# Optimization experiments

Hardware: AMD Instinct MI355X
Metric: run time of the kernel (lower is better)

Reference implementation:

```python
import jax, jax.numpy as jnp
import numpy as np

N, E, B, D, DEPTH = 20000, 160000, 16, 128, 5
L = 4 * DEPTH  # 20 EGNN layer calls: (ground, ground_to_sub, sub, sub_to_ground) x depth


def _ln(x, g, b):
    mu = jnp.mean(x, -1, keepdims=True)
    var = jnp.mean((x - mu) ** 2, -1, keepdims=True)
    return (x - mu) * jax.lax.rsqrt(var + 1e-5) * g + b


def setup_inputs() -> dict:
    key = jax.random.key(0)
    ks = jax.random.split(key, 24)

    def w(k, shape, fan_in):
        return jax.random.normal(k, shape, jnp.float32) / np.float32(np.sqrt(fan_in))

    return {
        "x": jax.random.normal(ks[0], (N, 1), jnp.float32),
        "pos": jax.random.normal(ks[1], (N, 3), jnp.float32),
        "edge_index": jax.random.randint(ks[2], (2, E), 0, N),
        "node_subnode_index": jax.random.randint(ks[3], (2, E), 0, N),
        "subgraph_edge_index": jax.random.randint(ks[4], (2, E), 0, N),
        "subnode_node_index": jax.random.randint(ks[5], (2, E), 0, N),
        "batch_ids": jnp.sort(jax.random.randint(ks[6], (N,), 0, B)),
        "emb_W": w(ks[7], (1, D), 1), "emb_b": jnp.zeros((D,), jnp.float32),
        # message MLP: Linear(2D+1,D) -> LN -> SiLU -> Linear(D,D) -> LN -> SiLU, stacked over L layers
        "Wm1": w(ks[8], (L, 2 * D + 1, D), 2 * D + 1), "bm1": jnp.zeros((L, D), jnp.float32),
        "gm1": jnp.ones((L, D), jnp.float32), "sm1": jnp.zeros((L, D), jnp.float32),
        "Wm2": w(ks[9], (L, D, D), D), "bm2": jnp.zeros((L, D), jnp.float32),
        "gm2": jnp.ones((L, D), jnp.float32), "sm2": jnp.zeros((L, D), jnp.float32),
        # update MLP: Linear(2D,D) -> LN -> SiLU -> Linear(D,D) -> LN -> SiLU
        "Wu1": w(ks[10], (L, 2 * D, D), 2 * D), "bu1": jnp.zeros((L, D), jnp.float32),
        "gu1": jnp.ones((L, D), jnp.float32), "su1": jnp.zeros((L, D), jnp.float32),
        "Wu2": w(ks[11], (L, D, D), D), "bu2": jnp.zeros((L, D), jnp.float32),
        "gu2": jnp.ones((L, D), jnp.float32), "su2": jnp.zeros((L, D), jnp.float32),
        # prediction head: Linear(D,D) -> ReLU -> Linear(D,1)
        "pred_W1": w(ks[12], (D, D), D), "pred_b1": jnp.zeros((D,), jnp.float32),
        "pred_W2": w(ks[13], (D, 1), D), "pred_b2": jnp.zeros((1,), jnp.float32),
    }


def _egnn(h, pos, ei, i, Wm1, bm1, gm1, sm1, Wm2, bm2, gm2, sm2,
          Wu1, bu1, gu1, su1, Wu2, bu2, gu2, su2):
    src, dst = ei[0], ei[1]          # PyG: messages flow source -> target
    rel = pos[dst] - pos[src]
    dist = jnp.sqrt(jnp.sum(rel * rel, -1, keepdims=True))  # [E,1]
    m = jnp.concatenate([h[dst], h[src], dist], -1)          # [E, 2D+1] = [h_i, h_j, d]
    m = jax.nn.silu(_ln(m @ Wm1[i] + bm1[i], gm1[i], sm1[i]))
    m = jax.nn.silu(_ln(m @ Wm2[i] + bm2[i], gm2[i], sm2[i]))
    agg = jax.ops.segment_sum(m, dst, num_segments=h.shape[0])
    u = jnp.concatenate([h, agg], -1)                        # [N, 2D]
    u = jax.nn.silu(_ln(u @ Wu1[i] + bu1[i], gu1[i], su1[i]))
    u = jax.nn.silu(_ln(u @ Wu2[i] + bu2[i], gu2[i], su2[i]))
    return u


def reference(x, pos, edge_index, node_subnode_index, subgraph_edge_index,
              subnode_node_index, batch_ids, emb_W, emb_b,
              Wm1, bm1, gm1, sm1, Wm2, bm2, gm2, sm2,
              Wu1, bu1, gu1, su1, Wu2, bu2, gu2, su2,
              pred_W1, pred_b1, pred_W2, pred_b2):
    p = (Wm1, bm1, gm1, sm1, Wm2, bm2, gm2, sm2,
         Wu1, bu1, gu1, su1, Wu2, bu2, gu2, su2)
    h = x @ emb_W + emb_b
    edge_sets = (edge_index, node_subnode_index, subgraph_edge_index, subnode_node_index)
    for layer_idx in range(DEPTH):
        h0 = h
        for r, ei in enumerate(edge_sets):
            h = _egnn(h, pos, ei, layer_idx * 4 + r, *p)
        h = h + h0  # residual across the 4 message-passing steps
    out = jax.ops.segment_sum(h, batch_ids, num_segments=B)  # global_add_pool
    return jax.nn.relu(out @ pred_W1 + pred_b1) @ pred_W2 + pred_b2
```

## Files before the change

### kernel.cpp

```cpp
#include <hip/hip_runtime.h>

#define NN 20000
#define NE 160000
#define NL 20

typedef float f32x4 __attribute__((ext_vector_type(4)));
typedef float f32x2 __attribute__((ext_vector_type(2)));
typedef __bf16 bf16x8 __attribute__((ext_vector_type(8)));
typedef __bf16 bf16x4 __attribute__((ext_vector_type(4)));

__device__ __forceinline__ float silu_f(float v) {
  return v * __builtin_amdgcn_rcpf(1.f + __expf(-v));
}

__global__ void pack_weights(const float* __restrict__ W, __bf16* __restrict__ out,
                             const int K, const int lstride, const int total) {
  const int idx = blockIdx.x * 256 + threadIdx.x;
  if (idx >= total) return;
  const int lane = idx & 63;
  const int nt = (idx >> 6) & 7;
  const int ktn = K >> 5;
  const int kt = (idx >> 9) % ktn;
  const int layer = (idx >> 9) / ktn;
  const int col = nt * 16 + (lane & 15);
  const int kb = kt * 32 + (lane >> 4) * 8;
  const float* src = W + (size_t)layer * lstride;
  __bf16* o = out + (size_t)idx * 8;
#pragma unroll
  for (int j = 0; j < 8; ++j) o[j] = (__bf16)src[(kb + j) * 128 + col];
}

__global__ void pack_w1pq(const float* __restrict__ Wm1, __bf16* __restrict__ out) {
  const int idx = blockIdx.x * 256 + threadIdx.x;
  const int lane = idx & 63;
  const int nt = (idx >> 6) & 15;
  const int kt = (idx >> 10) & 3;
  const int layer = idx >> 12;
  const int c = nt * 16 + (lane & 15);
  const int kb = kt * 32 + (lane >> 4) * 8;
  const float* src = Wm1 + (size_t)layer * 257 * 128;
  __bf16* o = out + (size_t)idx * 8;
#pragma unroll
  for (int j = 0; j < 8; ++j) {
    const int k = kb + j;
    o[j] = (__bf16)((c < 128) ? src[k * 128 + c] : src[(128 + k) * 128 + (c - 128)]);
  }
}

__global__ void embed_kernel(const float* __restrict__ x, const float* __restrict__ embW,
                             const float* __restrict__ embB,
                             float* __restrict__ h0, __bf16* __restrict__ hbf) {
  const int idx = blockIdx.x * 256 + threadIdx.x;
  const int n = idx >> 7, d = idx & 127;
  const float v = x[n] * embW[d] + embB[d];
  h0[idx] = v;
  hbf[idx] = (__bf16)v;
}

__global__ void hist_kernel(const int* __restrict__ ei, int* __restrict__ deg) {
  const int e = blockIdx.x * 256 + threadIdx.x;
  atomicAdd(&deg[ei[NE + e]], 1);
}

__global__ void scan_kernel(const int* __restrict__ deg, int* __restrict__ rowstart) {
  __shared__ int part[1024];
  const int r = blockIdx.x, t = threadIdx.x;
  const int* d = deg + (size_t)r * NN;
  int* rs = rowstart + (size_t)r * NN;
  int loc[20];
  int cnt = 0;
#pragma unroll
  for (int j = 0; j < 20; ++j) {
    const int i = t * 20 + j;
    const int v = (i < NN) ? d[i] : 0;
    loc[j] = cnt; cnt += v;
  }
  part[t] = cnt;
  __syncthreads();
  for (int off = 1; off < 1024; off <<= 1) {
    const int v = (t >= off) ? part[t - off] : 0;
    __syncthreads();
    part[t] += v;
    __syncthreads();
  }
  const int excl = (t == 0) ? 0 : part[t - 1];
#pragma unroll
  for (int j = 0; j < 20; ++j) {
    const int i = t * 20 + j;
    if (i < NN) rs[i] = excl + loc[j];
  }
}

__global__ void fill_kernel(const int* __restrict__ ei, const int* __restrict__ rowstart,
                            int* __restrict__ cursor, int* __restrict__ eord) {
  const int e = blockIdx.x * 256 + threadIdx.x;
  const int d = ei[NE + e];
  const int p = atomicAdd(&cursor[d], 1);
  eord[rowstart[d] + p] = e;
}

__global__ __launch_bounds__(256) void pq_kernel(
    const __bf16* __restrict__ hbf, const __bf16* __restrict__ pqw,
    __bf16* __restrict__ pq) {
  __shared__ __bf16 T1s[4][2048];
  const int t = threadIdx.x, w = t >> 6, l = t & 63;
  const int lr = l & 15, lg = l >> 4;
  const int wid = blockIdx.x * 4 + w;
  const int n0 = (wid >> 1) * 16;
  const int half = wid & 1;
  char* T1 = (char*)T1s[w];

  const int node = n0 + lr;
  bf16x8 bq[4];
#pragma unroll
  for (int kt = 0; kt < 4; ++kt)
    bq[kt] = *(const bf16x8*)(hbf + (size_t)node * 128 + kt * 32 + lg * 8);

  f32x4 acc[8];
#pragma unroll
  for (int nt = 0; nt < 8; ++nt) acc[nt] = (f32x4)0.f;
#pragma unroll
  for (int kt = 0; kt < 4; ++kt) {
#pragma unroll
    for (int nt = 0; nt < 8; ++nt) {
      const bf16x8 a = *(const bf16x8*)(pqw + ((size_t)((kt * 16 + half * 8 + nt) * 64 + l)) * 8);
      acc[nt] = __builtin_amdgcn_mfma_f32_16x16x32_bf16(a, bq[kt], acc[nt], 0, 0, 0);
    }
  }
#pragma unroll
  for (int nt = 0; nt < 8; ++nt) {
    bf16x4 v;
#pragma unroll
    for (int r = 0; r < 4; ++r) v[r] = (__bf16)acc[nt][r];
    *(bf16x4*)(T1 + ((lr * 256 + nt * 32 + lg * 8) ^ ((lr & 7) << 4))) = v;
  }
#pragma unroll
  for (int j = 0; j < 4; ++j) {
    const int row = j * 4 + lg;
    const uint4 v = *(const uint4*)(T1 + ((row * 256 + lr * 16) ^ ((row & 7) << 4)));
    *(uint4*)(pq + (size_t)(n0 + row) * 256 + half * 128 + lr * 8) = v;
  }
}

__global__ __launch_bounds__(512, 6) void edge_msg_kernel(
    const __bf16* __restrict__ pq, const float* __restrict__ pos,
    const int* __restrict__ ei, __bf16* __restrict__ msg,
    const __bf16* __restrict__ w2p, const float* __restrict__ w1last,
    const float* __restrict__ bm1, const float* __restrict__ gm1, const float* __restrict__ sm1,
    const float* __restrict__ bm2, const float* __restrict__ gm2, const float* __restrict__ sm2) {
  extern __shared__ char lds[];
  {
    const int t = threadIdx.x;
    uint4* d = (uint4*)lds;
    const uint4* s2 = (const uint4*)w2p;
#pragma unroll
    for (int j = 0; j < 4; ++j) d[t + j * 512] = s2[t + j * 512];
  }
  __syncthreads();

  const int t = threadIdx.x, w = t >> 6, l = t & 63;
  const int lr = l & 15, lg = l >> 4;
  char* W2L = lds;
  char* T1  = lds + 32768 + w * 2048;

  const int e0 = blockIdx.x * 128 + w * 16;
  const int es = ei[e0 + lr], ed = ei[NE + e0 + lr];
  const float dx = pos[ed * 3 + 0] - pos[es * 3 + 0];
  const float dy = pos[ed * 3 + 1] - pos[es * 3 + 1];
  const float dz = pos[ed * 3 + 2] - pos[es * 3 + 2];
  const float dist = sqrtf(dx * dx + dy * dy + dz * dz);

  float v[4][8];
#pragma unroll
  for (int kt = 0; kt < 4; ++kt) {
    const int d0 = kt * 32 + lg * 8;
    const bf16x8 pA = *(const bf16x8*)(pq + (size_t)ed * 256 + d0);
    const bf16x8 qA = *(const bf16x8*)(pq + (size_t)es * 256 + 128 + d0);
    const f32x4 wl0 = *(const f32x4*)(w1last + d0), wl1 = *(const f32x4*)(w1last + d0 + 4);
    const f32x4 bb0 = *(const f32x4*)(bm1 + d0),    bb1 = *(const f32x4*)(bm1 + d0 + 4);
#pragma unroll
    for (int j = 0; j < 4; ++j) {
      v[kt][j]     = (float)pA[j]     + (float)qA[j]     + dist * wl0[j] + bb0[j];
      v[kt][j + 4] = (float)pA[j + 4] + (float)qA[j + 4] + dist * wl1[j] + bb1[j];
    }
  }
  float s = 0.f, q = 0.f;
#pragma unroll
  for (int kt = 0; kt < 4; ++kt)
#pragma unroll
    for (int j = 0; j < 8; ++j) { const float x = v[kt][j]; s += x; q += x * x; }
  s += __shfl_xor(s, 16); q += __shfl_xor(q, 16);
  s += __shfl_xor(s, 32); q += __shfl_xor(q, 32);
  const float mu1 = s * 0.0078125f;
  const float rstd1 = rsqrtf(q * 0.0078125f - mu1 * mu1 + 1e-5f);
  bf16x8 bfrag[4];
#pragma unroll
  for (int kt = 0; kt < 4; ++kt) {
    const int d0 = kt * 32 + lg * 8;
    const f32x4 g0 = *(const f32x4*)(gm1 + d0), g1 = *(const f32x4*)(gm1 + d0 + 4);
    const f32x4 s0 = *(const f32x4*)(sm1 + d0), s1 = *(const f32x4*)(sm1 + d0 + 4);
    bf16x8 bf;
#pragma unroll
    for (int j = 0; j < 4; ++j) {
      bf[j]     = (__bf16)silu_f((v[kt][j]     - mu1) * rstd1 * g0[j] + s0[j]);
      bf[j + 4] = (__bf16)silu_f((v[kt][j + 4] - mu1) * rstd1 * g1[j] + s1[j]);
    }
    bfrag[kt] = bf;
  }
  f32x4 acc2[8];
#pragma unroll
  for (int nt = 0; nt < 8; ++nt)
    acc2[nt] = *(const f32x4*)(bm2 + nt * 16 + lg * 4);
#pragma unroll
  for (int kt = 0; kt < 4; ++kt) {
#pragma unroll
    for (int nt = 0; nt < 8; ++nt) {
      const bf16x8 a = *(const bf16x8*)(W2L + ((kt * 8 + nt) * 64 + l) * 16);
      acc2[nt] = __builtin_amdgcn_mfma_f32_16x16x32_bf16(a, bfrag[kt], acc2[nt], 0, 0, 0);
    }
  }
  float s2 = 0.f, q2 = 0.f;
#pragma unroll
  for (int nt = 0; nt < 8; ++nt)
#pragma unroll
    for (int r = 0; r < 4; ++r) { const float x = acc2[nt][r]; s2 += x; q2 += x * x; }
  s2 += __shfl_xor(s2, 16); q2 += __shfl_xor(q2, 16);
  s2 += __shfl_xor(s2, 32); q2 += __shfl_xor(q2, 32);
  const float mu2 = s2 * 0.0078125f;
  const float rstd2 = rsqrtf(q2 * 0.0078125f - mu2 * mu2 + 1e-5f);
#pragma unroll
  for (int hh = 0; hh < 2; ++hh) {
#pragma unroll
    for (int nt4 = 0; nt4 < 4; ++nt4) {
      const int nt = hh * 4 + nt4;
      const f32x4 g2 = *(const f32x4*)(gm2 + nt * 16 + lg * 4);
      const f32x4 b2 = *(const f32x4*)(sm2 + nt * 16 + lg * 4);
      bf16x4 pk;
#pragma unroll
      for (int r = 0; r < 4; ++r)
        pk[r] = (__bf16)silu_f((acc2[nt][r] - mu2) * rstd2 * g2[r] + b2[r]);
      *(bf16x4*)(T1 + ((lr * 128 + nt4 * 32 + lg * 8) ^ ((lr & 7) << 4))) = pk;
    }
#pragma unroll
    for (int j = 0; j < 2; ++j) {
      const int e8 = j * 8 + (l >> 3);
      const uint4 val = *(const uint4*)(T1 + ((e8 * 128 + (l & 7) * 16) ^ ((e8 & 7) << 4)));
      *(uint4*)((char*)msg + (size_t)(e0 + e8) * 256 + hh * 128 + (l & 7) * 16) = val;
    }
  }
}

__global__ void gather_kernel(const __bf16* __restrict__ msg,
                              const int* __restrict__ rowstart, const int* __restrict__ deg,
                              const int* __restrict__ eord, __bf16* __restrict__ aggb) {
  const int t = blockIdx.x * 256 + threadIdx.x;
  const int n = t >> 6, pd = t & 63;
  const int s = rowstart[n], dg = deg[n];
  float a0 = 0.f, a1 = 0.f;
  int i = 0;
  for (; i + 2 <= dg; i += 2) {
    const unsigned v0 = *(const unsigned*)(msg + (size_t)eord[s + i] * 128 + pd * 2);
    const unsigned v1 = *(const unsigned*)(msg + (size_t)eord[s + i + 1] * 128 + pd * 2);
    a0 += __uint_as_float(v0 << 16) + __uint_as_float(v1 << 16);
    a1 += __uint_as_float(v0 & 0xFFFF0000u) + __uint_as_float(v1 & 0xFFFF0000u);
  }
  if (i < dg) {
    const unsigned v0 = *(const unsigned*)(msg + (size_t)eord[s + i] * 128 + pd * 2);
    a0 += __uint_as_float(v0 << 16);
    a1 += __uint_as_float(v0 & 0xFFFF0000u);
  }
  __bf16 o0 = (__bf16)a0, o1 = (__bf16)a1;
  unsigned pk = ((unsigned)*(unsigned short*)&o0) | (((unsigned)*(unsigned short*)&o1) << 16);
  *(unsigned*)(aggb + (size_t)n * 128 + pd * 2) = pk;
}

__global__ __launch_bounds__(256) void update_kernel(
    float* __restrict__ h, const __bf16* __restrict__ aggb, __bf16* __restrict__ hbf,
    float* __restrict__ h0, const int mode,
    const __bf16* __restrict__ w1p, const __bf16* __restrict__ w2p,
    const float* __restrict__ bu1, const float* __restrict__ gu1, const float* __restrict__ su1,
    const float* __restrict__ bu2, const float* __restrict__ gu2, const float* __restrict__ su2) {
  __shared__ __bf16 T1s[4][16 * 128];
  const int t = threadIdx.x, w = t >> 6, l = t & 63;
  const int lr = l & 15, lg = l >> 4;
  char* T1 = (char*)T1s[w];
  const int n0 = blockIdx.x * 64 + w * 16;
  const int n = n0 + lr;
  const int valid = (n < NN);
  const int nc = valid ? n : 0;

  bf16x8 ah[4], af[4];
#pragma unroll
  for (int kt = 0; kt < 4; ++kt) {
    ah[kt] = *(const bf16x8*)(hbf + (size_t)nc * 128 + kt * 32 + lg * 8);
    af[kt] = *(const bf16x8*)(aggb + (size_t)nc * 128 + kt * 32 + lg * 8);
  }
  f32x4 acc[8];
#pragma unroll
  for (int nt = 0; nt < 8; ++nt) {
    const float bb = bu1[nt * 16 + lr];
#pragma unroll
    for (int r = 0; r < 4; ++r) acc[nt][r] = bb;
  }
#pragma unroll
  for (int kt = 0; kt < 8; ++kt) {
    const bf16x8 a = (kt < 4) ? ah[kt] : af[kt - 4];
#pragma unroll
    for (int nt = 0; nt < 8; ++nt) {
      const bf16x8 b = *(const bf16x8*)(w1p + ((size_t)((kt * 8 + nt) * 64 + l)) * 8);
      acc[nt] = __builtin_amdgcn_mfma_f32_16x16x32_bf16(a, b, acc[nt], 0, 0, 0);
    }
  }
  {
    float g1c[8], s1c[8];
#pragma unroll
    for (int nt = 0; nt < 8; ++nt) { g1c[nt] = gu1[nt * 16 + lr]; s1c[nt] = su1[nt * 16 + lr]; }
#pragma unroll
    for (int r = 0; r < 4; ++r) {
      float s = 0.f, q = 0.f;
#pragma unroll
      for (int nt = 0; nt < 8; ++nt) { const float v = acc[nt][r]; s += v; q += v * v; }
#pragma unroll
      for (int m = 1; m < 16; m <<= 1) { s += __shfl_xor(s, m); q += __shfl_xor(q, m); }
      const float mu = s * 0.0078125f;
      const float rstd = rsqrtf(q * 0.0078125f - mu * mu + 1e-5f);
      const int row = lg * 4 + r;
#pragma unroll
      for (int nt = 0; nt < 8; ++nt) {
        float v = (acc[nt][r] - mu) * rstd * g1c[nt] + s1c[nt];
        v = silu_f(v);
        const int col = nt * 16 + lr;
        *(__bf16*)(T1 + ((row * 256 + col * 2) ^ ((row & 7) << 4))) = (__bf16)v;
      }
    }
  }
  f32x4 acc2[8];
#pragma unroll
  for (int nt = 0; nt < 8; ++nt) {
    const float bb = bu2[nt * 16 + lr];
#pragma unroll
    for (int r = 0; r < 4; ++r) acc2[nt][r] = bb;
  }
#pragma unroll
  for (int kt = 0; kt < 4; ++kt) {
    const bf16x8 a = *(const bf16x8*)(T1 + ((lr * 256 + kt * 64 + lg * 16) ^ ((lr & 7) << 4)));
#pragma unroll
    for (int nt = 0; nt < 8; ++nt) {
      const bf16x8 b = *(const bf16x8*)(w2p + ((size_t)((kt * 8 + nt) * 64 + l)) * 8);
      acc2[nt] = __builtin_amdgcn_mfma_f32_16x16x32_bf16(a, b, acc2[nt], 0, 0, 0);
    }
  }
  {
    float g2c[8], s2c[8];
#pragma unroll
    for (int nt = 0; nt < 8; ++nt) { g2c[nt] = gu2[nt * 16 + lr]; s2c[nt] = su2[nt * 16 + lr]; }
#pragma unroll
    for (int r = 0; r < 4; ++r) {
      float s = 0.f, q = 0.f;
#pragma unroll
      for (int nt = 0; nt < 8; ++nt) { const float v = acc2[nt][r]; s += v; q += v * v; }
#pragma unroll
      for (int m = 1; m < 16; m <<= 1) { s += __shfl_xor(s, m); q += __shfl_xor(q, m); }
      const float mu = s * 0.0078125f;
      const float rstd = rsqrtf(q * 0.0078125f - mu * mu + 1e-5f);
      const int row = lg * 4 + r;
      const int nn = n0 + row;
      if (nn < NN) {
#pragma unroll
        for (int nt = 0; nt < 8; ++nt) {
          const int col = nt * 16 + lr;
          float v = (acc2[nt][r] - mu) * rstd * g2c[nt] + s2c[nt];
          v = silu_f(v);
          if (mode & 1) v += h0[(size_t)nn * 128 + col];
          if (mode & 2) {
            h[(size_t)nn * 128 + col] = v;
          } else {
            hbf[(size_t)nn * 128 + col] = (__bf16)v;
            if (mode & 1) h0[(size_t)nn * 128 + col] = v;
          }
        }
      }
    }
  }
}

__global__ void pool_kernel(const float* __restrict__ h, const int* __restrict__ bid,
                            float* __restrict__ pooled) {
  const int d = threadIdx.x;
  const int n0 = blockIdx.x * 32;
  const int nend = (n0 + 32 < NN) ? (n0 + 32) : NN;
  float acc = 0.f;
  int cur = bid[n0];
  for (int n = n0; n < nend; ++n) {
    const int b = bid[n];
    if (b != cur) { atomicAdd(&pooled[cur * 128 + d], acc); acc = 0.f; cur = b; }
    acc += h[(size_t)n * 128 + d];
  }
  atomicAdd(&pooled[cur * 128 + d], acc);
}

__global__ void head_kernel(const float* __restrict__ pooled,
                            const float* __restrict__ W1, const float* __restrict__ b1,
                            const float* __restrict__ W2, const float* __restrict__ b2,
                            float* __restrict__ out) {
  __shared__ float buf[2];
  const int b = blockIdx.x, t = threadIdx.x;
  float s = b1[t];
  for (int k = 0; k < 128; ++k) s += pooled[b * 128 + k] * W1[k * 128 + t];
  s = fmaxf(s, 0.f) * W2[t];
#pragma unroll
  for (int m = 32; m >= 1; m >>= 1) s += __shfl_down(s, m);
  if ((t & 63) == 0) buf[t >> 6] = s;
  __syncthreads();
  if (t == 0) out[b] = buf[0] + buf[1] + b2[0];
}

extern "C" void kernel_launch(void* const* d_in, const int* in_sizes, int n_in,
                              void* d_out, int out_size, void* d_ws, size_t ws_size,
                              hipStream_t stream) {
  const float* x   = (const float*)d_in[0];
  const float* pos = (const float*)d_in[1];
  const int* eis[4] = {(const int*)d_in[2], (const int*)d_in[3],
                       (const int*)d_in[4], (const int*)d_in[5]};
  const int* bid = (const int*)d_in[6];
  const float* embW = (const float*)d_in[7];
  const float* embB = (const float*)d_in[8];
  const float* Wm1 = (const float*)d_in[9];
  const float* bm1 = (const float*)d_in[10];
  const float* gm1 = (const float*)d_in[11];
  const float* sm1 = (const float*)d_in[12];
  const float* Wm2 = (const float*)d_in[13];
  const float* bm2 = (const float*)d_in[14];
  const float* gm2 = (const float*)d_in[15];
  const float* sm2 = (const float*)d_in[16];
  const float* Wu1 = (const float*)d_in[17];
  const float* bu1 = (const float*)d_in[18];
  const float* gu1 = (const float*)d_in[19];
  const float* su1 = (const float*)d_in[20];
  const float* Wu2 = (const float*)d_in[21];
  const float* bu2 = (const float*)d_in[22];
  const float* gu2 = (const float*)d_in[23];
  const float* su2 = (const float*)d_in[24];
  const float* pW1 = (const float*)d_in[25];
  const float* pb1 = (const float*)d_in[26];
  const float* pW2 = (const float*)d_in[27];
  const float* pb2 = (const float*)d_in[28];
  float* out = (float*)d_out;

  char* wp = (char*)d_ws;
  float* h = (float*)wp;      wp += (size_t)NN * 128 * 4;
  float* h0 = (float*)wp;     wp += (size_t)NN * 128 * 4;
  float* pooled = (float*)wp; wp += 16 * 128 * 4;
  __bf16* aggb = (__bf16*)wp; wp += (size_t)NN * 128 * 2;
  __bf16* hbf = (__bf16*)wp;  wp += (size_t)NN * 128 * 2;
  __bf16* pq = (__bf16*)wp;   wp += (size_t)NN * 256 * 2;
  __bf16* msg = (__bf16*)wp;  wp += (size_t)NE * 128 * 2;
  __bf16* pqw = (__bf16*)wp;  wp += (size_t)NL * 32768 * 2;
  __bf16* w2p = (__bf16*)wp;  wp += (size_t)NL * 16384 * 2;
  __bf16* wu1p = (__bf16*)wp; wp += (size_t)NL * 32768 * 2;
  __bf16* wu2p = (__bf16*)wp; wp += (size_t)NL * 16384 * 2;
  int* deg = (int*)wp;        wp += (size_t)4 * NN * 4;
  int* cursor = (int*)wp;     wp += (size_t)4 * NN * 4;
  int* rowstart = (int*)wp;   wp += (size_t)4 * NN * 4;
  int* eord = (int*)wp;       wp += (size_t)4 * NE * 4;

  static int lds_attr_set = 0;
  if (!lds_attr_set) {
    hipFuncSetAttribute((const void*)edge_msg_kernel,
                        hipFuncAttributeMaxDynamicSharedMemorySize, 49152);
    lds_attr_set = 1;
  }

  pack_w1pq<<<320, 256, 0, stream>>>(Wm1, pqw);
  pack_weights<<<160, 256, 0, stream>>>(Wm2, w2p, 128, 128 * 128, NL * 4 * 8 * 64);
  pack_weights<<<320, 256, 0, stream>>>(Wu1, wu1p, 256, 256 * 128, NL * 8 * 8 * 64);
  pack_weights<<<160, 256, 0, stream>>>(Wu2, wu2p, 128, 128 * 128, NL * 4 * 8 * 64);

  hipMemsetAsync(deg, 0, (size_t)8 * NN * 4, stream);
  embed_kernel<<<(NN * 128) / 256, 256, 0, stream>>>(x, embW, embB, h0, hbf);
  for (int r = 0; r < 4; ++r)
    hist_kernel<<<NE / 256, 256, 0, stream>>>(eis[r], deg + (size_t)r * NN);
  scan_kernel<<<4, 1024, 0, stream>>>(deg, rowstart);
  for (int r = 0; r < 4; ++r)
    fill_kernel<<<NE / 256, 256, 0, stream>>>(eis[r], rowstart + (size_t)r * NN,
                                              cursor + (size_t)r * NN, eord + (size_t)r * NE);

  for (int layer = 0; layer < 5; ++layer) {
    for (int r = 0; r < 4; ++r) {
      const int i = layer * 4 + r;
      const int mode = (r == 3) ? ((layer == 4) ? 3 : 1) : 0;
      pq_kernel<<<625, 256, 0, stream>>>(hbf, pqw + (size_t)i * 32768, pq);
      edge_msg_kernel<<<NE / 128, 512, 49152, stream>>>(
          pq, pos, eis[r], msg,
          w2p + (size_t)i * 16384,
          Wm1 + (size_t)i * 257 * 128 + 256 * 128,
          bm1 + i * 128, gm1 + i * 128, sm1 + i * 128,
          bm2 + i * 128, gm2 + i * 128, sm2 + i * 128);
      gather_kernel<<<(NN * 64) / 256, 256, 0, stream>>>(
          msg, rowstart + (size_t)r * NN, deg + (size_t)r * NN, eord + (size_t)r * NE, aggb);
      update_kernel<<<(NN + 63) / 64, 256, 0, stream>>>(
          h, aggb, hbf, h0, mode,
          wu1p + (size_t)i * 32768, wu2p + (size_t)i * 16384,
          bu1 + i * 128, gu1 + i * 128, su1 + i * 128,
          bu2 + i * 128, gu2 + i * 128, su2 + i * 128);
    }
  }

  hipMemsetAsync(pooled, 0, 16 * 128 * 4, stream);
  pool_kernel<<<(NN + 31) / 32, 128, 0, stream>>>(h, bid, pooled);
  head_kernel<<<16, 128, 0, stream>>>(pooled, pW1, pb1, pW2, pb2, out);
}
```

Baseline: 1.737 ms.

## Process edges in destination-sorted order so gather reads messages contiguously

The fill kernel now writes each edge's source and destination into CSR-sorted arrays instead of a permutation. The edge message kernel runs over edges in destination order, so messages land already grouped by destination. The gather kernel then sums a contiguous range of message rows without going through the indirection array. In exchange, destination-sorted order may change locality for the pq and pos gathers in the edge kernel, and the sum order depends on the atomics in fill, so results are not bitwise deterministic.

```diff
diff --git a/kernel.cpp b/kernel.cpp
--- a/kernel.cpp
+++ b/kernel.cpp
@@ -92,11 +92,14 @@
 }
 
 __global__ void fill_kernel(const int* __restrict__ ei, const int* __restrict__ rowstart,
-                            int* __restrict__ cursor, int* __restrict__ eord) {
+                            int* __restrict__ cursor,
+                            int* __restrict__ esrc, int* __restrict__ edst) {
   const int e = blockIdx.x * 256 + threadIdx.x;
+  const int sN = ei[e];
   const int d = ei[NE + e];
-  const int p = atomicAdd(&cursor[d], 1);
-  eord[rowstart[d] + p] = e;
+  const int p = rowstart[d] + atomicAdd(&cursor[d], 1);
+  esrc[p] = sN;
+  edst[p] = d;
 }
 
 __global__ __launch_bounds__(256) void pq_kernel(
@@ -144,7 +147,8 @@
 
 __global__ __launch_bounds__(512, 6) void edge_msg_kernel(
     const __bf16* __restrict__ pq, const float* __restrict__ pos,
-    const int* __restrict__ ei, __bf16* __restrict__ msg,
+    const int* __restrict__ esrc, const int* __restrict__ edst,
+    __bf16* __restrict__ msg,
     const __bf16* __restrict__ w2p, const float* __restrict__ w1last,
     const float* __restrict__ bm1, const float* __restrict__ gm1, const float* __restrict__ sm1,
     const float* __restrict__ bm2, const float* __restrict__ gm2, const float* __restrict__ sm2) {
@@ -164,7 +168,7 @@
   char* T1  = lds + 32768 + w * 2048;
 
   const int e0 = blockIdx.x * 128 + w * 16;
-  const int es = ei[e0 + lr], ed = ei[NE + e0 + lr];
+  const int es = esrc[e0 + lr], ed = edst[e0 + lr];
   const float dx = pos[ed * 3 + 0] - pos[es * 3 + 0];
   const float dy = pos[ed * 3 + 1] - pos[es * 3 + 1];
   const float dz = pos[ed * 3 + 2] - pos[es * 3 + 2];
@@ -252,20 +256,21 @@
 
 __global__ void gather_kernel(const __bf16* __restrict__ msg,
                               const int* __restrict__ rowstart, const int* __restrict__ deg,
-                              const int* __restrict__ eord, __bf16* __restrict__ aggb) {
+                              __bf16* __restrict__ aggb) {
   const int t = blockIdx.x * 256 + threadIdx.x;
   const int n = t >> 6, pd = t & 63;
   const int s = rowstart[n], dg = deg[n];
+  const char* base = (const char*)msg + (size_t)s * 256 + pd * 4;
   float a0 = 0.f, a1 = 0.f;
   int i = 0;
   for (; i + 2 <= dg; i += 2) {
-    const unsigned v0 = *(const unsigned*)(msg + (size_t)eord[s + i] * 128 + pd * 2);
-    const unsigned v1 = *(const unsigned*)(msg + (size_t)eord[s + i + 1] * 128 + pd * 2);
+    const unsigned v0 = *(const unsigned*)(base + (size_t)i * 256);
+    const unsigned v1 = *(const unsigned*)(base + (size_t)(i + 1) * 256);
     a0 += __uint_as_float(v0 << 16) + __uint_as_float(v1 << 16);
     a1 += __uint_as_float(v0 & 0xFFFF0000u) + __uint_as_float(v1 & 0xFFFF0000u);
   }
   if (i < dg) {
-    const unsigned v0 = *(const unsigned*)(msg + (size_t)eord[s + i] * 128 + pd * 2);
+    const unsigned v0 = *(const unsigned*)(base + (size_t)i * 256);
     a0 += __uint_as_float(v0 << 16);
     a1 += __uint_as_float(v0 & 0xFFFF0000u);
   }
@@ -462,7 +467,8 @@
   int* deg = (int*)wp;        wp += (size_t)4 * NN * 4;
   int* cursor = (int*)wp;     wp += (size_t)4 * NN * 4;
   int* rowstart = (int*)wp;   wp += (size_t)4 * NN * 4;
-  int* eord = (int*)wp;       wp += (size_t)4 * NE * 4;
+  int* esrc = (int*)wp;       wp += (size_t)4 * NE * 4;
+  int* edst = (int*)wp;       wp += (size_t)4 * NE * 4;
 
   static int lds_attr_set = 0;
   if (!lds_attr_set) {
@@ -483,7 +489,8 @@
   scan_kernel<<<4, 1024, 0, stream>>>(deg, rowstart);
   for (int r = 0; r < 4; ++r)
     fill_kernel<<<NE / 256, 256, 0, stream>>>(eis[r], rowstart + (size_t)r * NN,
-                                              cursor + (size_t)r * NN, eord + (size_t)r * NE);
+                                              cursor + (size_t)r * NN,
+                                              esrc + (size_t)r * NE, edst + (size_t)r * NE);
 
   for (int layer = 0; layer < 5; ++layer) {
     for (int r = 0; r < 4; ++r) {
@@ -491,13 +498,13 @@
       const int mode = (r == 3) ? ((layer == 4) ? 3 : 1) : 0;
       pq_kernel<<<625, 256, 0, stream>>>(hbf, pqw + (size_t)i * 32768, pq);
       edge_msg_kernel<<<NE / 128, 512, 49152, stream>>>(
-          pq, pos, eis[r], msg,
+          pq, pos, esrc + (size_t)r * NE, edst + (size_t)r * NE, msg,
           w2p + (size_t)i * 16384,
           Wm1 + (size_t)i * 257 * 128 + 256 * 128,
           bm1 + i * 128, gm1 + i * 128, sm1 + i * 128,
           bm2 + i * 128, gm2 + i * 128, sm2 + i * 128);
       gather_kernel<<<(NN * 64) / 256, 256, 0, stream>>>(
-          msg, rowstart + (size_t)r * NN, deg + (size_t)r * NN, eord + (size_t)r * NE, aggb);
+          msg, rowstart + (size_t)r * NN, deg + (size_t)r * NN, aggb);
       update_kernel<<<(NN + 63) / 64, 256, 0, stream>>>(
           h, aggb, hbf, h0, mode,
           wu1p + (size_t)i * 32768, wu2p + (size_t)i * 16384,
```

After: 1.570 ms (median of 2 runs). 1.11x faster.
